# Performance work log

Measured on AMD Instinct MI355X. Metric: run time of the kernel, lower is better.

## Reference

```python
import jax, jax.numpy as jnp
from jax import lax
import numpy as np

NUM_KIND = 4
V, H, B = 34, 32, 4096   # raw vertical (2 rows dropped), horizontal, batch
KS = 33                  # odd-rounded max(V-2, H)
NUM_DEPTH = 4
N_SQ = 100


def _conv(x, w):
    # x: (N,1,h,w), w: (1,1,KS,KS); torch Conv2d == cross-correlation == lax default
    return lax.conv_general_dilated(x, w, (1, 1), 'SAME',
                                    dimension_numbers=('NCHW', 'OIHW', 'NCHW'))


def _conv_k(x, w):
    # x: (K,B,1,h,w) -> conv each map with the shared 1-channel kernel
    k, b, c, h, wd = x.shape
    return _conv(x.reshape(k * b, c, h, wd), w).reshape(k, b, c, h, wd)


def setup_inputs() -> dict:
    key = jax.random.key(0)
    ks = jax.random.split(key, 8)
    std = 0.3
    return {
        'dots':    jax.random.randint(ks[0], (V, H, B), 0, NUM_KIND + 1, dtype=jnp.int32),
        'w_each':  jax.random.normal(ks[1], (1, 1, KS, KS), jnp.float32) * std,
        'w_not':   jax.random.normal(ks[2], (1, 1, KS, KS), jnp.float32) * std,
        'w_not2':  jax.random.normal(ks[3], (1, 1, KS, KS), jnp.float32) * std,
        'w_empty': jax.random.normal(ks[4], (1, 1, KS, KS), jnp.float32) * std,
        'W1':      jax.random.normal(ks[5], (N_SQ, (V - 2) * H), jnp.float32) * std,
        'W2':      jax.random.normal(ks[6], (N_SQ, N_SQ), jnp.float32) * std,
        'W3':      jax.random.normal(ks[7], (1, N_SQ), jnp.float32) * std,
    }


def reference(dots, w_each, w_not, w_not2, w_empty, W1, W2, W3):
    # drop last 2 vertical rows, layout (V-2,H,B) -> (B,1,V-2,H)
    board = dots[:-2].astype(jnp.float32).transpose(2, 0, 1)[:, None]  # (B,1,h,w)

    empty = (board == 0).astype(jnp.float32)
    E = _conv(empty, w_empty)                                           # (B,1,h,w)

    kinds = jnp.arange(1, NUM_KIND + 1, dtype=board.dtype).reshape(NUM_KIND, 1, 1, 1, 1)
    each = (board[None] == kinds).astype(jnp.float32)                   # (K,B,1,h,w)
    notm = ((each + empty[None]) == 0).astype(jnp.float32)              # (K,B,1,h,w)

    # first pass: per-color value, masked to that color's cells
    notm_conv = _conv_k(notm, w_not)      # note: the torch code LOGS the convolved not-mask
    v = _conv_k(each, w_each) + E[None] - notm_conv
    L = each * v                          # each_color_value_log (masked)
    s = jax.nn.sigmoid(L.sum(axis=0))     # all_color_value_2nd, (B,1,h,w)

    # iterative diffusion; torch mutates the log in-place each depth:
    # L <- mask * (L + E + conv2nd(notm_conv * before)); before is detached
    for _ in range(NUM_DEPTH):
        before = lax.stop_gradient(s)
        C = _conv_k(notm_conv * before[None], w_not2)
        L = each * (L + E[None] + C)
        s = jax.nn.sigmoid(L.sum(axis=0))

    feat = s.reshape(s.shape[0], -1)      # (B, (V-2)*H)
    x = jax.nn.leaky_relu(feat @ W1.T, 0.2)
    x = jax.nn.leaky_relu(x @ W2.T, 0.2)
    return x @ W3.T                        # (B,1)
```

## Files before the change

kernel.cpp:

```cpp
#include <hip/hip_runtime.h>
#include <cstdint>
#include <cstddef>


typedef _Float16 f16;
typedef __attribute__((ext_vector_type(8))) _Float16 f16x8;
typedef __attribute__((ext_vector_type(4))) float f32x4;

#define NB   4096
#define PIX  1024
#define MR   (NB * 4)

__device__ __forceinline__ void gld_lds16(const void* g, void* l) {
    __builtin_amdgcn_global_load_lds(
        (const __attribute__((address_space(1))) void*)g,
        (__attribute__((address_space(3))) void*)l, 16, 0, 0);
}

__global__ void build_mats(const float* __restrict__ we, const float* __restrict__ wn,
                           const float* __restrict__ wn2, const float* __restrict__ wem,
                           f16* __restrict__ Me, f16* __restrict__ Mn,
                           f16* __restrict__ Mn2, f16* __restrict__ Mem) {
    int idx = blockIdx.x * 256 + threadIdx.x;
    int o = idx >> 10, in = idx & 1023;
    int i = o >> 5, j = o & 31, a = in >> 5, b = in & 31;
    int u = a - i + 16, v = b - j + 16;
    bool ok = (u >= 0) && (u < 33) && (v >= 0) && (v < 33);
    int w = u * 33 + v;
    float ve = 0.f, vn = 0.f, vn2 = 0.f, vem = 0.f;
    if (ok) { ve = we[w]; vn = wn[w]; vn2 = wn2[w]; vem = wem[w]; }
    Me[idx]  = (f16)ve;
    Mn[idx]  = (f16)vn;
    Mn2[idx] = (f16)vn2;
    Mem[idx] = (f16)vem;
}

__global__ void build_w1(const float* __restrict__ W1, f16* __restrict__ W1b) {
    int idx = blockIdx.x * 256 + threadIdx.x;
    int j = idx >> 10, i = idx & 1023;
    W1b[idx] = (f16)(j < 100 ? W1[j * 1024 + i] : 0.f);
}

__global__ void build_board(const int* __restrict__ dots, unsigned char* __restrict__ board) {
    __shared__ unsigned char tile[64][68];
    int t = threadIdx.x;
    int bp = blockIdx.x & 15, bn = blockIdx.x >> 4;
    int p0 = bp * 64, n0 = bn * 64;
    int ln = t & 63, lp = t >> 6;
#pragma unroll
    for (int j = 0; j < 16; j++) {
        int p = lp * 16 + j;
        tile[p][ln] = (unsigned char)dots[(size_t)(p0 + p) * 4096 + n0 + ln];
    }
    __syncthreads();
#pragma unroll
    for (int j = 0; j < 16; j++) {
        int n = lp * 16 + j;
        board[(size_t)(n0 + n) * 1024 + p0 + ln] = tile[ln][n];
    }
}

__global__ void mk_sa(const f16* __restrict__ S1sel, const f16* __restrict__ En,
                      const f16* __restrict__ NC,
                      const unsigned char* __restrict__ board,
                      float* __restrict__ Lsel, f16* __restrict__ P1) {
    int idx = blockIdx.x * 256 + threadIdx.x;
    int n = idx >> 10, o = idx & 1023;
    int c = board[idx];
    size_t r0 = (size_t)(4 * n) * PIX + o;
    f16 nc0 = NC[r0], nc1 = NC[r0 + PIX], nc2 = NC[r0 + 2 * PIX], nc3 = NC[r0 + 3 * PIX];
    float L = 0.f;
    if (c > 0) {
        float ncsel = (float)((c == 1) ? nc0 : (c == 2) ? nc1 : (c == 3) ? nc2 : nc3);
        L = (float)S1sel[idx] + (float)En[idx] - ncsel;
    }
    Lsel[idx] = L;
    f16 s = (f16)(1.f / (1.f + __expf(-L)));
    P1[r0]           = nc0 * s;
    P1[r0 + PIX]     = nc1 * s;
    P1[r0 + 2 * PIX] = nc2 * s;
    P1[r0 + 3 * PIX] = nc3 * s;
}

template <int MODE, int ASRC>
__device__ __forceinline__ void run_gemm(
    int bjob, int ypx, int nx, char* smem,
    const f16* __restrict__ X, const f16* __restrict__ B,
    const unsigned char* __restrict__ board,
    f16* __restrict__ outB, int ldo, float* __restrict__ outF) {
    char* smB = smem;
    char* smA = smem + 16384;

    const int tid = threadIdx.x;
    const int wv = tid >> 6, ln = tid & 63;
    const int wm = wv >> 1, wn_ = wv & 1;
    const int lr = ln & 15, lq = ln >> 4;

    int xcd = bjob & 7, slot = bjob >> 3;
    int bx = slot % nx;
    int by = xcd * ypx + slot / nx;
    const int rtile = by * 128, otile = bx * 128;
    const int img0 = (ASRC == 4) ? rtile : (rtile >> 2);

    const f32x4 fz = {0.f, 0.f, 0.f, 0.f};
    f32x4 acc[4][4];
#pragma unroll
    for (int i = 0; i < 4; i++)
#pragma unroll
        for (int j = 0; j < 4; j++) acc[i][j] = fz;

    for (int kb = 0; kb < 1024; kb += 64) {
#pragma unroll
        for (int t = 0; t < 4; t++) {
            int c = (wv * 4 + t) * 64 + ln;
            int row = c >> 3, gcol = (c & 7) ^ (row & 7);
            gld_lds16(B + (size_t)(otile + row) * 1024 + kb + gcol * 8, smB + c * 16);
        }
        if (ASRC == 0) {
#pragma unroll
            for (int t = 0; t < 4; t++) {
                int c = (wv * 4 + t) * 64 + ln;
                int row = c >> 3, gcol = (c & 7) ^ (row & 7);
                gld_lds16(X + (size_t)(rtile + row) * 1024 + kb + gcol * 8, smA + c * 16);
            }
        } else if (ASRC == 4) {
#pragma unroll
            for (int t = 0; t < 2; t++) {
                int c = t * 256 + wv * 64 + ln;
                int row = c >> 2, g = (c & 3) ^ (row & 3);
                gld_lds16(board + (size_t)(img0 + row) * 1024 + kb + g * 16, smA + c * 16);
            }
        } else {
            if (wv < 2) {
                int c = wv * 64 + ln;
                int row = c >> 2, g = (c & 3) ^ (row & 3);
                gld_lds16(board + (size_t)(img0 + row) * 1024 + kb + g * 16, smA + c * 16);
            }
        }
        __syncthreads();

#pragma unroll
        for (int kk = 0; kk < 2; kk++) {
            const int oct = kk * 4 + lq;
            f16x8 af[4], bfr[4];
#pragma unroll
            for (int i = 0; i < 4; i++) {
                int rrow = wm * 64 + i * 16 + lr;
                if (ASRC == 0) {
                    af[i] = *(const f16x8*)(smA + rrow * 128 + (oct ^ (rrow & 7)) * 16);
                } else {
                    int m = (ASRC == 4) ? rrow : (rrow >> 2);
                    int k1 = (rrow & 3) + 1;
                    uint64_t bb = *(const uint64_t*)(smA + m * 64 +
                                    ((oct >> 1) ^ (m & 3)) * 16 + (oct & 1) * 8);
                    f16x8 v;
#pragma unroll
                    for (int jj = 0; jj < 8; jj++) {
                        int bj = (int)((bb >> (8 * jj)) & 0xff);
                        bool on = (ASRC == 2) ? (bj == k1)
                                : (ASRC == 3) ? (bj != 0 && bj != k1)
                                              : (bj == 0);
                        v[jj] = on ? (f16)1.f : (f16)0.f;
                    }
                    af[i] = v;
                }
            }
#pragma unroll
            for (int j = 0; j < 4; j++) {
                int brow = wn_ * 64 + j * 16 + lr;
                bfr[j] = *(const f16x8*)(smB + brow * 128 + (oct ^ (brow & 7)) * 16);
            }
#pragma unroll
            for (int i = 0; i < 4; i++)
#pragma unroll
                for (int j = 0; j < 4; j++)
                    acc[i][j] = __builtin_amdgcn_mfma_f32_16x16x32_f16(
                        af[i], bfr[j], acc[i][j], 0, 0, 0);
        }
        __syncthreads();
    }

#pragma unroll
    for (int i = 0; i < 4; i++) {
        int rbase = rtile + wm * 64 + i * 16 + lq * 4;
#pragma unroll
        for (int j = 0; j < 4; j++) {
            int o = otile + wn_ * 64 + j * 16 + lr;
            f32x4 a = acc[i][j];
            if (MODE == 0) {
#pragma unroll
                for (int v = 0; v < 4; v++)
                    outB[(size_t)(rbase + v) * ldo + o] = (f16)a[v];
            } else if (MODE == 5) {
#pragma unroll
                for (int v = 0; v < 4; v++) {
                    float x = a[v];
                    outF[(size_t)(rbase + v) * ldo + o] = x > 0.f ? x : 0.2f * x;
                }
            } else {
                int n = rbase >> 2;
                size_t no = (size_t)n * PIX + o;
                int c = board[no];
                float asel = (c == 1) ? a[0] : (c == 2) ? a[1] : (c == 3) ? a[2] : a[3];
                outB[no] = (f16)asel;
            }
        }
    }
}

__global__ void __launch_bounds__(256, 4) gemm_fa(
    const f16* __restrict__ Me, const f16* __restrict__ Mn,
    const f16* __restrict__ Mem, const unsigned char* __restrict__ board,
    f16* __restrict__ S1sel, f16* __restrict__ NC, f16* __restrict__ En) {
    __shared__ __attribute__((aligned(16))) char smem[24576];
    int bi = blockIdx.x;
    if (bi < 1024) {
        run_gemm<1, 2>(bi, 16, 8, smem, nullptr, Me, board, S1sel, 0, nullptr);
    } else if (bi < 2048) {
        run_gemm<0, 3>(bi - 1024, 16, 8, smem, nullptr, Mn, board, NC, PIX, nullptr);
    } else {
        run_gemm<0, 4>(bi - 2048, 4, 8, smem, nullptr, Mem, board, En, PIX, nullptr);
    }
}

template <int MODE>
__global__ void __launch_bounds__(256, 2) gemm_depth(
    const f16* __restrict__ Pin, const f16* __restrict__ Mn2,
    const unsigned char* __restrict__ board, const f16* __restrict__ NC,
    const f16* __restrict__ En, float* __restrict__ Lsel,
    f16* __restrict__ Pout, f16* __restrict__ feat) {
    __shared__ __attribute__((aligned(16))) char smem[32768];
    char* smB = smem;
    char* smA = smem + 16384;

    const int tid = threadIdx.x;
    const int wv = tid >> 6, ln = tid & 63;
    const int wm = wv >> 1, wn_ = wv & 1;
    const int lr = ln & 15, lq = ln >> 4;

    int bi = blockIdx.x;
    int xcd = bi & 7, slot = bi >> 3;
    int bx = slot & 7;
    int by = xcd * 16 + (slot >> 3);
    const int rtile = by * 128, otile = bx * 128;

    const f32x4 fz = {0.f, 0.f, 0.f, 0.f};
    f32x4 acc[4][4];
#pragma unroll
    for (int i = 0; i < 4; i++)
#pragma unroll
        for (int j = 0; j < 4; j++) acc[i][j] = fz;

    for (int kb = 0; kb < 1024; kb += 64) {
#pragma unroll
        for (int t = 0; t < 4; t++) {
            int c = (wv * 4 + t) * 64 + ln;
            int row = c >> 3, gcol = (c & 7) ^ (row & 7);
            gld_lds16(Mn2 + (size_t)(otile + row) * 1024 + kb + gcol * 8, smB + c * 16);
            gld_lds16(Pin + (size_t)(rtile + row) * 1024 + kb + gcol * 8, smA + c * 16);
        }
        __syncthreads();

#pragma unroll
        for (int kk = 0; kk < 2; kk++) {
            const int oct = kk * 4 + lq;
            f16x8 af[4], bfr[4];
#pragma unroll
            for (int i = 0; i < 4; i++) {
                int rrow = wm * 64 + i * 16 + lr;
                af[i] = *(const f16x8*)(smA + rrow * 128 + (oct ^ (rrow & 7)) * 16);
            }
#pragma unroll
            for (int j = 0; j < 4; j++) {
                int brow = wn_ * 64 + j * 16 + lr;
                bfr[j] = *(const f16x8*)(smB + brow * 128 + (oct ^ (brow & 7)) * 16);
            }
#pragma unroll
            for (int i = 0; i < 4; i++)
#pragma unroll
                for (int j = 0; j < 4; j++)
                    acc[i][j] = __builtin_amdgcn_mfma_f32_16x16x32_f16(
                        af[i], bfr[j], acc[i][j], 0, 0, 0);
        }
        __syncthreads();
    }

#pragma unroll
    for (int i = 0; i < 4; i++) {
        int rbase = rtile + wm * 64 + i * 16 + lq * 4;
#pragma unroll
        for (int j = 0; j < 4; j++) {
            int o = otile + wn_ * 64 + j * 16 + lr;
            f32x4 a = acc[i][j];
            int n = rbase >> 2;
            size_t no = (size_t)n * PIX + o;
            int c = board[no];
            float asel = (c == 1) ? a[0] : (c == 2) ? a[1] : (c == 3) ? a[2] : a[3];
            float E = (float)En[no];
            float Lnew = (c > 0) ? (Lsel[no] + E + asel) : 0.f;
            float s = 1.f / (1.f + __expf(-Lnew));
            if (MODE == 4) {
                feat[no] = (f16)s;
            } else {
                Lsel[no] = Lnew;
                f16 sh = (f16)s;
                size_t r0 = (size_t)rbase * PIX + o;
                Pout[r0]           = NC[r0] * sh;
                Pout[r0 + PIX]     = NC[r0 + PIX] * sh;
                Pout[r0 + 2 * PIX] = NC[r0 + 2 * PIX] * sh;
                Pout[r0 + 3 * PIX] = NC[r0 + 3 * PIX] * sh;
            }
        }
    }
}

__global__ void __launch_bounds__(256, 4) gemm_mlp(
    const f16* __restrict__ feat, const f16* __restrict__ W1b,
    float* __restrict__ X1) {
    __shared__ __attribute__((aligned(16))) char smem[32768];
    run_gemm<5, 0>(blockIdx.x, 4, 1, smem, feat, W1b, nullptr, nullptr, 128, X1);
}

__global__ void __launch_bounds__(256) mlp23(const float* __restrict__ X1,
                                             const float* __restrict__ W2,
                                             const float* __restrict__ W3,
                                             float* __restrict__ out) {
    __shared__ float sW2[10000];
    __shared__ float sW3[100];
    __shared__ float red[256];
    int t = threadIdx.x;
    for (int idx = t; idx < 10000; idx += 256) sW2[idx] = W2[idx];
    if (t < 100) sW3[t] = W3[t];
    __syncthreads();
    int nb = t >> 2, q = t & 3;
    int n = blockIdx.x * 64 + nb;
    const float* x1 = X1 + (size_t)n * 128;
    float xr[100];
#pragma unroll
    for (int i = 0; i < 100; i++) xr[i] = x1[i];
    float partial = 0.f;
    for (int jj = 0; jj < 25; jj++) {
        int j = q + jj * 4;
        const float* w2r = sW2 + j * 100;
        float acc2 = 0.f;
#pragma unroll
        for (int i = 0; i < 100; i++) acc2 += w2r[i] * xr[i];
        partial += sW3[j] * (acc2 > 0.f ? acc2 : 0.2f * acc2);
    }
    red[t] = partial;
    __syncthreads();
    if (q == 0) out[n] = red[t] + red[t + 1] + red[t + 2] + red[t + 3];
}

extern "C" void kernel_launch(void* const* d_in, const int* in_sizes, int n_in,
                              void* d_out, int out_size, void* d_ws, size_t ws_size,
                              hipStream_t stream) {
    (void)in_sizes; (void)n_in; (void)out_size; (void)ws_size;
    const int*   dots   = (const int*)d_in[0];
    const float* w_each = (const float*)d_in[1];
    const float* w_not  = (const float*)d_in[2];
    const float* w_not2 = (const float*)d_in[3];
    const float* w_emp  = (const float*)d_in[4];
    const float* W1 = (const float*)d_in[5];
    const float* W2 = (const float*)d_in[6];
    const float* W3 = (const float*)d_in[7];
    float* out = (float*)d_out;

    char* ws = (char*)d_ws;
    size_t off = 0;
    auto alloc = [&](size_t bytes) -> char* {
        char* p = ws + off;
        off += (bytes + 255) & ~(size_t)255;
        return p;
    };
    f16* Me    = (f16*)alloc((size_t)PIX * PIX * 2);
    f16* Mn    = (f16*)alloc((size_t)PIX * PIX * 2);
    f16* Mn2   = (f16*)alloc((size_t)PIX * PIX * 2);
    f16* Mem   = (f16*)alloc((size_t)PIX * PIX * 2);
    f16* W1b   = (f16*)alloc((size_t)128 * PIX * 2);
    unsigned char* board = (unsigned char*)alloc((size_t)NB * PIX);
    f16* NC    = (f16*)alloc((size_t)MR * PIX * 2);
    f16* En    = (f16*)alloc((size_t)NB * PIX * 2);
    f16* S1sel = (f16*)alloc((size_t)NB * PIX * 2);
    f16* Pa    = (f16*)alloc((size_t)MR * PIX * 2);
    f16* Pb    = (f16*)alloc((size_t)MR * PIX * 2);
    f16* feat  = (f16*)alloc((size_t)NB * PIX * 2);
    float* Lsel= (float*)alloc((size_t)NB * PIX * 4);
    float* X1  = (float*)alloc((size_t)NB * 128 * 4);

    build_board<<<1024, 256, 0, stream>>>(dots, board);
    build_mats<<<4096, 256, 0, stream>>>(w_each, w_not, w_not2, w_emp,
                                         Me, Mn, Mn2, Mem);
    build_w1<<<512, 256, 0, stream>>>(W1, W1b);

    dim3 blk(256);
    gemm_fa<<<2304, blk, 0, stream>>>(Me, Mn, Mem, board, S1sel, NC, En);
    mk_sa<<<16384, blk, 0, stream>>>(S1sel, En, NC, board, Lsel, Pa);
    gemm_depth<3><<<1024, blk, 0, stream>>>(Pa, Mn2, board, NC, En, Lsel, Pb, nullptr);
    gemm_depth<3><<<1024, blk, 0, stream>>>(Pb, Mn2, board, NC, En, Lsel, Pa, nullptr);
    gemm_depth<3><<<1024, blk, 0, stream>>>(Pa, Mn2, board, NC, En, Lsel, Pb, nullptr);
    gemm_depth<4><<<1024, blk, 0, stream>>>(Pb, Mn2, board, NC, En, Lsel, nullptr, feat);
    gemm_mlp<<<32, blk, 0, stream>>>(feat, W1b, X1);
    mlp23<<<64, blk, 0, stream>>>(X1, W2, W3, out);
}
```

Before: 417.9 us.

## Merge setup kernels, fuse MLP layers, store Lsel in half precision

```diff
diff --git a/kernel.cpp b/kernel.cpp
--- a/kernel.cpp
+++ b/kernel.cpp
@@ -17,53 +17,54 @@
         (__attribute__((address_space(3))) void*)l, 16, 0, 0);
 }
 
-__global__ void build_mats(const float* __restrict__ we, const float* __restrict__ wn,
-                           const float* __restrict__ wn2, const float* __restrict__ wem,
-                           f16* __restrict__ Me, f16* __restrict__ Mn,
-                           f16* __restrict__ Mn2, f16* __restrict__ Mem) {
-    int idx = blockIdx.x * 256 + threadIdx.x;
-    int o = idx >> 10, in = idx & 1023;
-    int i = o >> 5, j = o & 31, a = in >> 5, b = in & 31;
-    int u = a - i + 16, v = b - j + 16;
-    bool ok = (u >= 0) && (u < 33) && (v >= 0) && (v < 33);
-    int w = u * 33 + v;
-    float ve = 0.f, vn = 0.f, vn2 = 0.f, vem = 0.f;
-    if (ok) { ve = we[w]; vn = wn[w]; vn2 = wn2[w]; vem = wem[w]; }
-    Me[idx]  = (f16)ve;
-    Mn[idx]  = (f16)vn;
-    Mn2[idx] = (f16)vn2;
-    Mem[idx] = (f16)vem;
-}
-
-__global__ void build_w1(const float* __restrict__ W1, f16* __restrict__ W1b) {
-    int idx = blockIdx.x * 256 + threadIdx.x;
-    int j = idx >> 10, i = idx & 1023;
-    W1b[idx] = (f16)(j < 100 ? W1[j * 1024 + i] : 0.f);
-}
-
-__global__ void build_board(const int* __restrict__ dots, unsigned char* __restrict__ board) {
+__global__ void build_all(const float* __restrict__ we, const float* __restrict__ wn,
+                          const float* __restrict__ wn2, const float* __restrict__ wem,
+                          const float* __restrict__ W1, const int* __restrict__ dots,
+                          f16* __restrict__ Me, f16* __restrict__ Mn,
+                          f16* __restrict__ Mn2, f16* __restrict__ Mem,
+                          f16* __restrict__ W1b, unsigned char* __restrict__ board) {
     __shared__ unsigned char tile[64][68];
-    int t = threadIdx.x;
-    int bp = blockIdx.x & 15, bn = blockIdx.x >> 4;
-    int p0 = bp * 64, n0 = bn * 64;
-    int ln = t & 63, lp = t >> 6;
-#pragma unroll
-    for (int j = 0; j < 16; j++) {
-        int p = lp * 16 + j;
-        tile[p][ln] = (unsigned char)dots[(size_t)(p0 + p) * 4096 + n0 + ln];
-    }
-    __syncthreads();
-#pragma unroll
-    for (int j = 0; j < 16; j++) {
-        int n = lp * 16 + j;
-        board[(size_t)(n0 + n) * 1024 + p0 + ln] = tile[ln][n];
+    int bi = blockIdx.x, t = threadIdx.x;
+    if (bi < 4096) {
+        int idx = bi * 256 + t;
+        int o = idx >> 10, in = idx & 1023;
+        int i = o >> 5, j = o & 31, a = in >> 5, b = in & 31;
+        int u = a - i + 16, v = b - j + 16;
+        bool ok = (u >= 0) && (u < 33) && (v >= 0) && (v < 33);
+        int w = u * 33 + v;
+        float ve = 0.f, vn = 0.f, vn2 = 0.f, vem = 0.f;
+        if (ok) { ve = we[w]; vn = wn[w]; vn2 = wn2[w]; vem = wem[w]; }
+        Me[idx]  = (f16)ve;
+        Mn[idx]  = (f16)vn;
+        Mn2[idx] = (f16)vn2;
+        Mem[idx] = (f16)vem;
+    } else if (bi < 4608) {
+        int idx = (bi - 4096) * 256 + t;
+        int j = idx >> 10, i = idx & 1023;
+        W1b[idx] = (f16)(j < 100 ? W1[j * 1024 + i] : 0.f);
+    } else {
+        int bb = bi - 4608;
+        int bp = bb & 15, bn = bb >> 4;
+        int p0 = bp * 64, n0 = bn * 64;
+        int ln = t & 63, lp = t >> 6;
+#pragma unroll
+        for (int j = 0; j < 16; j++) {
+            int p = lp * 16 + j;
+            tile[p][ln] = (unsigned char)dots[(size_t)(p0 + p) * 4096 + n0 + ln];
+        }
+        __syncthreads();
+#pragma unroll
+        for (int j = 0; j < 16; j++) {
+            int n = lp * 16 + j;
+            board[(size_t)(n0 + n) * 1024 + p0 + ln] = tile[ln][n];
+        }
     }
 }
 
 __global__ void mk_sa(const f16* __restrict__ S1sel, const f16* __restrict__ En,
                       const f16* __restrict__ NC,
                       const unsigned char* __restrict__ board,
-                      float* __restrict__ Lsel, f16* __restrict__ P1) {
+                      f16* __restrict__ Lsel, f16* __restrict__ P1) {
     int idx = blockIdx.x * 256 + threadIdx.x;
     int n = idx >> 10, o = idx & 1023;
     int c = board[idx];
@@ -74,7 +75,7 @@
         float ncsel = (float)((c == 1) ? nc0 : (c == 2) ? nc1 : (c == 3) ? nc2 : nc3);
         L = (float)S1sel[idx] + (float)En[idx] - ncsel;
     }
-    Lsel[idx] = L;
+    Lsel[idx] = (f16)L;
     f16 s = (f16)(1.f / (1.f + __expf(-L)));
     P1[r0]           = nc0 * s;
     P1[r0 + PIX]     = nc1 * s;
@@ -87,7 +88,7 @@
     int bjob, int ypx, int nx, char* smem,
     const f16* __restrict__ X, const f16* __restrict__ B,
     const unsigned char* __restrict__ board,
-    f16* __restrict__ outB, int ldo, float* __restrict__ outF) {
+    f16* __restrict__ outB, int ldo) {
     char* smB = smem;
     char* smA = smem + 16384;
 
@@ -191,12 +192,6 @@
 #pragma unroll
                 for (int v = 0; v < 4; v++)
                     outB[(size_t)(rbase + v) * ldo + o] = (f16)a[v];
-            } else if (MODE == 5) {
-#pragma unroll
-                for (int v = 0; v < 4; v++) {
-                    float x = a[v];
-                    outF[(size_t)(rbase + v) * ldo + o] = x > 0.f ? x : 0.2f * x;
-                }
             } else {
                 int n = rbase >> 2;
                 size_t no = (size_t)n * PIX + o;
@@ -215,11 +210,11 @@
     __shared__ __attribute__((aligned(16))) char smem[24576];
     int bi = blockIdx.x;
     if (bi < 1024) {
-        run_gemm<1, 2>(bi, 16, 8, smem, nullptr, Me, board, S1sel, 0, nullptr);
+        run_gemm<1, 2>(bi, 16, 8, smem, nullptr, Me, board, S1sel, 0);
     } else if (bi < 2048) {
-        run_gemm<0, 3>(bi - 1024, 16, 8, smem, nullptr, Mn, board, NC, PIX, nullptr);
+        run_gemm<0, 3>(bi - 1024, 16, 8, smem, nullptr, Mn, board, NC, PIX);
     } else {
-        run_gemm<0, 4>(bi - 2048, 4, 8, smem, nullptr, Mem, board, En, PIX, nullptr);
+        run_gemm<0, 4>(bi - 2048, 4, 8, smem, nullptr, Mem, board, En, PIX);
     }
 }
 
@@ -227,7 +222,7 @@
 __global__ void __launch_bounds__(256, 2) gemm_depth(
     const f16* __restrict__ Pin, const f16* __restrict__ Mn2,
     const unsigned char* __restrict__ board, const f16* __restrict__ NC,
-    const f16* __restrict__ En, float* __restrict__ Lsel,
+    const f16* __restrict__ En, f16* __restrict__ Lsel,
     f16* __restrict__ Pout, f16* __restrict__ feat) {
     __shared__ __attribute__((aligned(16))) char smem[32768];
     char* smB = smem;
@@ -297,12 +292,12 @@
             int c = board[no];
             float asel = (c == 1) ? a[0] : (c == 2) ? a[1] : (c == 3) ? a[2] : a[3];
             float E = (float)En[no];
-            float Lnew = (c > 0) ? (Lsel[no] + E + asel) : 0.f;
+            float Lnew = (c > 0) ? ((float)Lsel[no] + E + asel) : 0.f;
             float s = 1.f / (1.f + __expf(-Lnew));
             if (MODE == 4) {
                 feat[no] = (f16)s;
             } else {
-                Lsel[no] = Lnew;
+                Lsel[no] = (f16)Lnew;
                 f16 sh = (f16)s;
                 size_t r0 = (size_t)rbase * PIX + o;
                 Pout[r0]           = NC[r0] * sh;
@@ -314,42 +309,104 @@
     }
 }
 
-__global__ void __launch_bounds__(256, 4) gemm_mlp(
+__global__ void __launch_bounds__(256) gemm_mlp_fused(
     const f16* __restrict__ feat, const f16* __restrict__ W1b,
-    float* __restrict__ X1) {
-    __shared__ __attribute__((aligned(16))) char smem[32768];
-    run_gemm<5, 0>(blockIdx.x, 4, 1, smem, feat, W1b, nullptr, nullptr, 128, X1);
-}
-
-__global__ void __launch_bounds__(256) mlp23(const float* __restrict__ X1,
-                                             const float* __restrict__ W2,
-                                             const float* __restrict__ W3,
-                                             float* __restrict__ out) {
-    __shared__ float sW2[10000];
-    __shared__ float sW3[100];
-    __shared__ float red[256];
-    int t = threadIdx.x;
-    for (int idx = t; idx < 10000; idx += 256) sW2[idx] = W2[idx];
-    if (t < 100) sW3[t] = W3[t];
-    __syncthreads();
-    int nb = t >> 2, q = t & 3;
-    int n = blockIdx.x * 64 + nb;
-    const float* x1 = X1 + (size_t)n * 128;
-    float xr[100];
-#pragma unroll
-    for (int i = 0; i < 100; i++) xr[i] = x1[i];
-    float partial = 0.f;
-    for (int jj = 0; jj < 25; jj++) {
-        int j = q + jj * 4;
-        const float* w2r = sW2 + j * 100;
-        float acc2 = 0.f;
-#pragma unroll
-        for (int i = 0; i < 100; i++) acc2 += w2r[i] * xr[i];
-        partial += sW3[j] * (acc2 > 0.f ? acc2 : 0.2f * acc2);
-    }
-    red[t] = partial;
-    __syncthreads();
-    if (q == 0) out[n] = red[t] + red[t + 1] + red[t + 2] + red[t + 3];
+    const float* __restrict__ W2, const float* __restrict__ W3,
+    float* __restrict__ out) {
+    __shared__ __attribute__((aligned(16))) char smem[47360];
+    char* smB = smem;
+    char* smA = smem + 16384;
+
+    const int tid = threadIdx.x;
+    const int wv = tid >> 6, ln = tid & 63;
+    const int wm = wv >> 1, wn_ = wv & 1;
+    const int lr = ln & 15, lq = ln >> 4;
+    const int rtile = blockIdx.x * 128;
+
+    const f32x4 fz = {0.f, 0.f, 0.f, 0.f};
+    f32x4 acc[4][4];
+#pragma unroll
+    for (int i = 0; i < 4; i++)
+#pragma unroll
+        for (int j = 0; j < 4; j++) acc[i][j] = fz;
+
+    for (int kb = 0; kb < 1024; kb += 64) {
+#pragma unroll
+        for (int t = 0; t < 4; t++) {
+            int c = (wv * 4 + t) * 64 + ln;
+            int row = c >> 3, gcol = (c & 7) ^ (row & 7);
+            gld_lds16(W1b  + (size_t)row * 1024 + kb + gcol * 8, smB + c * 16);
+            gld_lds16(feat + (size_t)(rtile + row) * 1024 + kb + gcol * 8, smA + c * 16);
+        }
+        __syncthreads();
+#pragma unroll
+        for (int kk = 0; kk < 2; kk++) {
+            const int oct = kk * 4 + lq;
+            f16x8 af[4], bfr[4];
+#pragma unroll
+            for (int i = 0; i < 4; i++) {
+                int rrow = wm * 64 + i * 16 + lr;
+                af[i] = *(const f16x8*)(smA + rrow * 128 + (oct ^ (rrow & 7)) * 16);
+            }
+#pragma unroll
+            for (int j = 0; j < 4; j++) {
+                int brow = wn_ * 64 + j * 16 + lr;
+                bfr[j] = *(const f16x8*)(smB + brow * 128 + (oct ^ (brow & 7)) * 16);
+            }
+#pragma unroll
+            for (int i = 0; i < 4; i++)
+#pragma unroll
+                for (int j = 0; j < 4; j++)
+                    acc[i][j] = __builtin_amdgcn_mfma_f32_16x16x32_f16(
+                        af[i], bfr[j], acc[i][j], 0, 0, 0);
+        }
+        __syncthreads();
+    }
+
+    float* xs  = (float*)smem;
+    f16*   sW2 = (f16*)(smem + 25856);
+    float* sW3 = (float*)(smem + 45856);
+    float* red = (float*)(smem + 46272);
+    for (int idx = tid; idx < 10000; idx += 256) sW2[idx] = (f16)W2[idx];
+    if (tid < 100) sW3[tid] = W3[tid];
+
+    for (int half = 0; half < 2; half++) {
+        if (wm == half) {
+#pragma unroll
+            for (int i = 0; i < 4; i++) {
+                int rb = i * 16 + lq * 4;
+#pragma unroll
+                for (int j = 0; j < 4; j++) {
+                    int o = wn_ * 64 + j * 16 + lr;
+                    if (o < 100) {
+                        f32x4 a = acc[i][j];
+#pragma unroll
+                        for (int v = 0; v < 4; v++) {
+                            float x = a[v];
+                            xs[(rb + v) * 101 + o] = x > 0.f ? x : 0.2f * x;
+                        }
+                    }
+                }
+            }
+        }
+        __syncthreads();
+        int nb = tid >> 2, q = tid & 3;
+        const float* xrow = xs + nb * 101;
+        float partial = 0.f;
+        for (int jj = 0; jj < 25; jj++) {
+            int j = q + jj * 4;
+            const f16* w2r = sW2 + j * 100;
+            float a2 = 0.f;
+#pragma unroll
+            for (int i = 0; i < 100; i++) a2 += (float)w2r[i] * xrow[i];
+            partial += sW3[j] * (a2 > 0.f ? a2 : 0.2f * a2);
+        }
+        red[tid] = partial;
+        __syncthreads();
+        if (q == 0)
+            out[rtile + half * 64 + nb] = red[tid] + red[tid + 1] + red[tid + 2] + red[tid + 3];
+        __syncthreads();
+    }
 }
 
 extern "C" void kernel_launch(void* const* d_in, const int* in_sizes, int n_in,
@@ -385,21 +442,16 @@
     f16* Pa    = (f16*)alloc((size_t)MR * PIX * 2);
     f16* Pb    = (f16*)alloc((size_t)MR * PIX * 2);
     f16* feat  = (f16*)alloc((size_t)NB * PIX * 2);
-    float* Lsel= (float*)alloc((size_t)NB * PIX * 4);
-    float* X1  = (float*)alloc((size_t)NB * 128 * 4);
-
-    build_board<<<1024, 256, 0, stream>>>(dots, board);
-    build_mats<<<4096, 256, 0, stream>>>(w_each, w_not, w_not2, w_emp,
-                                         Me, Mn, Mn2, Mem);
-    build_w1<<<512, 256, 0, stream>>>(W1, W1b);
+    f16* Lsel  = (f16*)alloc((size_t)NB * PIX * 2);
 
     dim3 blk(256);
+    build_all<<<5632, blk, 0, stream>>>(w_each, w_not, w_not2, w_emp, W1, dots,
+                                        Me, Mn, Mn2, Mem, W1b, board);
     gemm_fa<<<2304, blk, 0, stream>>>(Me, Mn, Mem, board, S1sel, NC, En);
     mk_sa<<<16384, blk, 0, stream>>>(S1sel, En, NC, board, Lsel, Pa);
     gemm_depth<3><<<1024, blk, 0, stream>>>(Pa, Mn2, board, NC, En, Lsel, Pb, nullptr);
     gemm_depth<3><<<1024, blk, 0, stream>>>(Pb, Mn2, board, NC, En, Lsel, Pa, nullptr);
     gemm_depth<3><<<1024, blk, 0, stream>>>(Pa, Mn2, board, NC, En, Lsel, Pb, nullptr);
     gemm_depth<4><<<1024, blk, 0, stream>>>(Pb, Mn2, board, NC, En, Lsel, nullptr, feat);
-    gemm_mlp<<<32, blk, 0, stream>>>(feat, W1b, X1);
-    mlp23<<<64, blk, 0, stream>>>(X1, W2, W3, out);
-}
+    gemm_mlp_fused<<<32, blk, 0, stream>>>(feat, W1b, W2, W3, out);
+}
```

Measured after the change: 410.4 us. Within noise of the previous version (-1.8%).
